# Kernel optimization log

Hardware: AMD Instinct MI355X
Metric: run time of the kernel (lower is better)

## Reference

```python
import jax, jax.numpy as jnp
import numpy as np

ENC = 512   # ENCODER_DIM / card embedding size / LSTM input size
CTX = 512   # context_embeddings width
H = 512     # LSTM hidden size
N = 100000  # num_cards


def _lstm_step(x, h, c, w_ih, w_hh, b_ih, b_hh):
    # PyTorch LSTM gate order: i, f, g, o
    gates = x @ w_ih.T + b_ih + h @ w_hh.T + b_hh
    i, f, g, o = jnp.split(gates, 4, axis=-1)
    c_new = jax.nn.sigmoid(f) * c + jax.nn.sigmoid(i) * jnp.tanh(g)
    h_new = jax.nn.sigmoid(o) * jnp.tanh(c_new)
    return h_new, c_new


def setup_inputs() -> dict:
    key = jax.random.key(0)
    ks = jax.random.split(key, 16)
    s = 0.05
    f32 = jnp.float32
    return {
        "context_embeddings": jax.random.normal(ks[0], (1, CTX), f32),
        "card_embeddings": jax.random.normal(ks[1], (N, ENC), f32),
        "eos_embedding": jax.random.normal(ks[2], (ENC,), f32) * 0.1,
        "ctx_w": jax.random.normal(ks[3], (ENC, CTX), f32) * s,
        "ctx_b": jnp.zeros((ENC,), f32),
        "out_w": jax.random.normal(ks[4], (ENC, H), f32) * s,
        "out_b": jnp.zeros((ENC,), f32),
        "w_ih_0": jax.random.normal(ks[5], (4 * H, ENC), f32) * s,
        "w_hh_0": jax.random.normal(ks[6], (4 * H, H), f32) * s,
        "b_ih_0": jnp.zeros((4 * H,), f32),
        "b_hh_0": jnp.zeros((4 * H,), f32),
        "w_ih_1": jax.random.normal(ks[7], (4 * H, H), f32) * s,
        "w_hh_1": jax.random.normal(ks[8], (4 * H, H), f32) * s,
        "b_ih_1": jnp.zeros((4 * H,), f32),
        "b_hh_1": jnp.zeros((4 * H,), f32),
        "max_selections": 5,
    }


def reference(context_embeddings, card_embeddings, eos_embedding,
              ctx_w, ctx_b, out_w, out_b,
              w_ih_0, w_hh_0, b_ih_0, b_hh_0,
              w_ih_1, w_hh_1, b_ih_1, b_hh_1,
              max_selections):
    temperature = 1.0
    num_cards = card_embeddings.shape[0]
    hid = w_hh_0.shape[1]
    dt = card_embeddings.dtype

    # initial LSTM step on projected context with zero state (seq_len == 1)
    x0 = context_embeddings @ ctx_w.T + ctx_b                     # [1, ENC]
    z = jnp.zeros((1, hid), dt)
    h0, c0 = _lstm_step(x0, z, z, w_ih_0, w_hh_0, b_ih_0, b_hh_0)
    h1, c1 = _lstm_step(h0, z, z, w_ih_1, w_hh_1, b_ih_1, b_hh_1)

    all_emb = jnp.concatenate([card_embeddings, eos_embedding[None, :]], axis=0)  # [N+1, ENC]
    avail = jnp.ones((num_cards,), bool)
    active = jnp.array(True)
    total_log_prob = jnp.asarray(0.0, dt)
    keys = jax.random.split(jax.random.key(42), max_selections)
    card_ids = jnp.arange(num_cards)

    indices = []
    n_steps = min(int(max_selections), num_cards)
    for step in range(n_steps):
        proj = h1 @ out_w.T + out_b                               # [1, ENC]
        card_sims = proj @ card_embeddings.T                      # [1, N]
        eos_sim = proj @ eos_embedding[:, None]                   # [1, 1]
        logits = jnp.concatenate([card_sims, eos_sim], axis=-1)[0] / temperature  # [N+1]
        ext_mask = jnp.concatenate([avail, jnp.ones((1,), bool)])
        logits = jnp.where(ext_mask, logits, -jnp.inf)

        idx = jax.random.categorical(keys[step], logits)          # multinomial(softmax(logits))
        log_prob = jax.nn.log_softmax(logits)[idx]
        total_log_prob = total_log_prob + jnp.where(active, log_prob, jnp.asarray(0.0, dt))

        is_eos = idx == num_cards
        take = active & (~is_eos)
        indices.append(jnp.where(take, idx, -1).astype(jnp.int32))
        avail = avail & ~((card_ids == idx) & take)

        # straight-through one-hot gather of the selected embedding
        hard = jax.nn.one_hot(idx, num_cards + 1, dtype=dt)
        soft = jax.nn.softmax(logits)
        ste = hard + soft - jax.lax.stop_gradient(soft)
        sel_emb = (ste @ all_emb)[None, :]                        # [1, ENC]

        h0, c0 = _lstm_step(sel_emb, h0, c0, w_ih_0, w_hh_0, b_ih_0, b_hh_0)
        h1, c1 = _lstm_step(h0, h1, c1, w_ih_1, w_hh_1, b_ih_1, b_hh_1)
        active = active & (~is_eos)

    selected_indices = jnp.stack(indices)                         # [max_selections], -1 = not selected
    return selected_indices, total_log_prob
```

## Files before the change

### kernel.cpp

```cpp
#include <hip/hip_runtime.h>
#include <stdint.h>
#include <math.h>

#define ENC 512
#define NSTEPS 5
#define NBLK 512
#define NTHR 256
#define NWAVES ((NBLK * NTHR) / 64)
#define ROWS_PER_ITER (NWAVES * 8)
#define FB_BLOCKS 1024
#define FB_WAVES (FB_BLOCKS * 256 / 64)
#define GSTRIDE 100032

struct SelState {
  int   taken[8];
  int   takenCount;
  int   active;
  int   outIdx[8];
  float tlp;
};

struct KParams {
  const float *ctx, *cards, *eos, *ctx_w, *ctx_b, *out_w, *out_b;
  const float *w_ih_0, *w_hh_0, *b_ih_0, *b_hh_0;
  const float *w_ih_1, *w_hh_1, *b_ih_1, *b_hh_1;
  unsigned* bar;
  float* xbuf;
  float* h0s; float* c0s; float* h1s; float* c1s;
  float* projs;
  SelState* st;
  float* bScore; int* bIdxA; float* bLogit; float* bM; float* bS;
  float* gtab;
  float* out;
  int ncards;
  uint32_t k0[NSTEPS], k1[NSTEPS];
};

__host__ __device__ __forceinline__ void tf2x32(uint32_t k0, uint32_t k1,
                                                uint32_t x0, uint32_t x1,
                                                uint32_t& o0, uint32_t& o1) {
  uint32_t ks0 = k0, ks1 = k1, ks2 = k0 ^ k1 ^ 0x1BD11BDAu;
  uint32_t ks[3] = {ks0, ks1, ks2};
  const uint32_t R0[4] = {13u, 15u, 26u, 6u};
  const uint32_t R1[4] = {17u, 29u, 16u, 24u};
  x0 += ks0; x1 += ks1;
#pragma unroll
  for (int i = 0; i < 5; ++i) {
    const uint32_t* r = (i & 1) ? R1 : R0;
#pragma unroll
    for (int j = 0; j < 4; ++j) {
      x0 += x1;
      x1 = (x1 << r[j]) | (x1 >> (32u - r[j]));
      x1 ^= x0;
    }
    x0 += ks[(i + 1) % 3];
    x1 += ks[(i + 2) % 3] + (uint32_t)(i + 1);
  }
  o0 = x0; o1 = x1;
}

__device__ __forceinline__ float gumbel_from_bits(uint32_t bits) {
  float f = __uint_as_float((bits >> 9) | 0x3F800000u) - 1.0f;
  float u = (f == 0.0f) ? 1.17549435e-38f : f;
  return -logf(-logf(u));
}

__device__ __forceinline__ float xla_tanh(float x) {
  if (fabsf(x) < 0.0004f) return x;
  const float kLim = 7.90531110763549805f;
  float cx = fminf(fmaxf(x, -kLim), kLim);
  float x2 = cx * cx;
  float p = -2.76076847742355e-16f;
  p = fmaf(p, x2, 2.00018790482477e-13f);
  p = fmaf(p, x2, -8.60467152213735e-11f);
  p = fmaf(p, x2, 5.12229709037114e-08f);
  p = fmaf(p, x2, 1.48572235717979e-05f);
  p = fmaf(p, x2, 6.37261928875436e-04f);
  p = fmaf(p, x2, 4.89352455891786e-03f);
  p = cx * p;
  float q = 1.19825839466702e-06f;
  q = fmaf(q, x2, 1.18534705686654e-04f);
  q = fmaf(q, x2, 2.26843463243900e-03f);
  q = fmaf(q, x2, 4.89352518554385e-03f);
  return p / q;
}
__device__ __forceinline__ float xla_sigmoid(float x) {
  return 0.5f * xla_tanh(0.5f * x) + 0.5f;
}

__device__ __forceinline__ float dot8(const float4* a, const float4* b, int lane) {
  float4 x0 = a[lane * 2], x1 = a[lane * 2 + 1];
  float4 y0 = b[lane * 2], y1 = b[lane * 2 + 1];
  return x0.x * y0.x + x0.y * y0.y + x0.z * y0.z + x0.w * y0.w +
         x1.x * y1.x + x1.y * y1.y + x1.z * y1.z + x1.w * y1.w;
}
__device__ __forceinline__ float wred(float v) {
#pragma unroll
  for (int k = 1; k < 64; k <<= 1) v += __shfl_xor(v, k, 64);
  return v;
}

__device__ __forceinline__ void cstoref(float* p, float v) {
  __hip_atomic_store(p, v, __ATOMIC_RELAXED, __HIP_MEMORY_SCOPE_AGENT);
}
__device__ __forceinline__ void cstorei(int* p, int v) {
  __hip_atomic_store(p, v, __ATOMIC_RELAXED, __HIP_MEMORY_SCOPE_AGENT);
}

__device__ __forceinline__ void arrive(unsigned* bar, int bid, unsigned target) {
  asm volatile("s_waitcnt vmcnt(0)" ::: "memory");
  __syncthreads();
  if (threadIdx.x == 0)
    __hip_atomic_store(&bar[(unsigned)bid * 16u], target,
                       __ATOMIC_RELAXED, __HIP_MEMORY_SCOPE_AGENT);
}
__device__ __forceinline__ void waitall(unsigned* bar, unsigned target) {
  const int tid = threadIdx.x;
  unsigned* s0 = &bar[(2u * (unsigned)tid) * 16u];
  unsigned* s1 = &bar[(2u * (unsigned)tid + 1u) * 16u];
  while (__hip_atomic_load(s0, __ATOMIC_RELAXED, __HIP_MEMORY_SCOPE_AGENT) < target)
    __builtin_amdgcn_s_sleep(1);
  while (__hip_atomic_load(s1, __ATOMIC_RELAXED, __HIP_MEMORY_SCOPE_AGENT) < target)
    __builtin_amdgcn_s_sleep(1);
  __syncthreads();
}
__device__ __forceinline__ void gsync(unsigned* bar, int bid, unsigned target) {
  arrive(bar, bid, target);
  waitall(bar, target);
}

__device__ __forceinline__ void lstm_phase(const float* wih, const float* whh,
                                           const float* bih, const float* bhh,
                                           const float* x, const float* hin, const float* cin,
                                           float* hout, float* cout, float* sG,
                                           int bid, int tid) {
  if (bid < ENC) {
    int g = tid >> 6, lane = tid & 63;
    size_t row = (size_t)(g * ENC + bid) * ENC;
    float accI = dot8((const float4*)(wih + row), (const float4*)x, lane);
    float accH = 0.0f;
    if (hin) accH = dot8((const float4*)(whh + row), (const float4*)hin, lane);
#pragma unroll
    for (int k = 1; k < 64; k <<= 1) {
      accI += __shfl_xor(accI, k, 64);
      accH += __shfl_xor(accH, k, 64);
    }
    if (lane == 0) sG[g] = ((accI + bih[g * ENC + bid]) + accH) + bhh[g * ENC + bid];
    __syncthreads();
    if (tid == 0) {
      float gi = sG[0], gf = sG[1], gg = sG[2], go = sG[3];
      float cprev = cin ? cin[bid] : 0.0f;
      float cn = xla_sigmoid(gf) * cprev + xla_sigmoid(gi) * xla_tanh(gg);
      float hn = xla_sigmoid(go) * xla_tanh(cn);
      cstoref(&cout[bid], cn);
      cstoref(&hout[bid], hn);
    }
  }
}

__global__ __launch_bounds__(NTHR, 2) void mega(KParams P) {
  const int bid = blockIdx.x, tid = threadIdx.x;
  const int wid = tid >> 6, lane = tid & 63;
  const int gw = bid * 4 + wid;
  const int sub = lane & 15;
  const int grp = lane >> 4;
  const int g = wid;
  unsigned ph = 0;

  __shared__ float sG[4];
  __shared__ float fS[NTHR], fL[NTHR], fM[NTHR], fU[NTHR];
  __shared__ int   fI[NTHR];
  __shared__ float wSs[16], wLs[16], wMs[16], wUs[16];
  __shared__ int   wIs[16];
  __shared__ int   sTaken[8];
  __shared__ int   sActive;
  __shared__ float sTlp;
  __shared__ int   sOut[NSTEPS];
  __shared__ int   selSh;

  if (tid == 0) {
    for (int i = 0; i < 8; ++i) sTaken[i] = -1;
    sActive = 1; sTlp = 0.0f;
    for (int i = 0; i < NSTEPS; ++i) sOut[i] = -1;
  }

  const int np1 = P.ncards + 1;
  const int ITERS = (np1 + ROWS_PER_ITER - 1) / ROWS_PER_ITER;

  {
    int total = NSTEPS * np1;
    for (int j = bid * NTHR + tid; j < total; j += NBLK * NTHR) {
      int s = j / np1;
      int i = j - s * np1;
      uint32_t r0, r1;
      tf2x32(P.k0[s], P.k1[s], 0u, (uint32_t)i, r0, r1);
      cstoref(&P.gtab[s * GSTRIDE + i], gumbel_from_bits(r0 ^ r1));
    }
  }
  if (gw >= NWAVES - ENC) {
    int r = gw - (NWAVES - ENC);
    float acc = wred(dot8((const float4*)(P.ctx_w + (size_t)r * ENC), (const float4*)P.ctx, lane));
    if (lane == 0) cstoref(&P.xbuf[r], acc + P.ctx_b[r]);
  }
  gsync(P.bar, bid, ++ph);

  lstm_phase(P.w_ih_0, P.w_hh_0, P.b_ih_0, P.b_hh_0, P.xbuf, nullptr, nullptr,
             P.h0s, P.c0s, sG, bid, tid);
  gsync(P.bar, bid, ++ph);
  lstm_phase(P.w_ih_1, P.w_hh_1, P.b_ih_1, P.b_hh_1, P.h0s, nullptr, nullptr,
             P.h1s, P.c1s, sG, bid, tid);
  gsync(P.bar, bid, ++ph);

  if (gw < ENC) {
    float acc = wred(dot8((const float4*)(P.out_w + (size_t)gw * ENC), (const float4*)P.h1s, lane));
    if (lane == 0) cstoref(&P.projs[gw], acc + P.out_b[gw]);
  }
  gsync(P.bar, bid, ++ph);

  for (int s = 0; s < NSTEPS; ++s) {
    {
      const float4* pv = (const float4*)(P.projs + s * ENC);
      float4 pr[8];
#pragma unroll
      for (int k = 0; k < 8; ++k) pr[k] = pv[sub + 16 * k];
      int t0 = sTaken[0], t1 = sTaken[1], t2 = sTaken[2], t3 = sTaken[3], t4 = sTaken[4];
      const float* gt = P.gtab + s * GSTRIDE;
      float bSc = -INFINITY, bLg = 0.0f, m = -INFINITY, su = 0.0f;
      int bIx = 0x7FFFFFFF;
      for (int t = 0; t < ITERS; ++t) {
        int base = (t * NWAVES + gw) * 8;
        int rA = base + grp;
        int rB = base + 4 + grp;
        bool vA = (rA < np1), vB = (rB < np1);
        const float* rpA = vA ? ((rA < P.ncards) ? (P.cards + (size_t)rA * ENC) : P.eos) : P.cards;
        const float* rpB = vB ? ((rB < P.ncards) ? (P.cards + (size_t)rB * ENC) : P.eos) : P.cards;
        const float4* ra = (const float4*)rpA;
        const float4* rb = (const float4*)rpB;
        float4 rrA[8], rrB[8];
#pragma unroll
        for (int k = 0; k < 8; ++k) { rrA[k] = ra[sub + 16 * k]; rrB[k] = rb[sub + 16 * k]; }
        float gA = vA ? gt[rA] : 0.0f;
        float gB = vB ? gt[rB] : 0.0f;
        float accA = 0.0f, accB = 0.0f;
#pragma unroll
        for (int k = 0; k < 8; ++k) {
          accA += rrA[k].x * pr[k].x + rrA[k].y * pr[k].y + rrA[k].z * pr[k].z + rrA[k].w * pr[k].w;
          accB += rrB[k].x * pr[k].x + rrB[k].y * pr[k].y + rrB[k].z * pr[k].z + rrB[k].w * pr[k].w;
        }
        accA += __shfl_xor(accA, 1, 64); accB += __shfl_xor(accB, 1, 64);
        accA += __shfl_xor(accA, 2, 64); accB += __shfl_xor(accB, 2, 64);
        accA += __shfl_xor(accA, 4, 64); accB += __shfl_xor(accB, 4, 64);
        accA += __shfl_xor(accA, 8, 64); accB += __shfl_xor(accB, 8, 64);
        if (sub == 0) {
          if (vA) {
            bool masked = (rA < P.ncards) &&
                          (rA == t0 || rA == t1 || rA == t2 || rA == t3 || rA == t4);
            if (!masked) {
              if (accA > m) { su = su * expf(m - accA) + 1.0f; m = accA; }
              else          { su += expf(accA - m); }
              float score = gA + accA;
              if (score > bSc || (score == bSc && rA < bIx)) { bSc = score; bIx = rA; bLg = accA; }
            }
          }
          if (vB) {
            bool masked = (rB < P.ncards) &&
                          (rB == t0 || rB == t1 || rB == t2 || rB == t3 || rB == t4);
            if (!masked) {
              if (accB > m) { su = su * expf(m - accB) + 1.0f; m = accB; }
              else          { su += expf(accB - m); }
              float score = gB + accB;
              if (score > bSc || (score == bSc && rB < bIx)) { bSc = score; bIx = rB; bLg = accB; }
            }
          }
        }
      }
      if (sub == 0) {
        int q = wid * 4 + grp;
        wSs[q] = bSc; wIs[q] = bIx; wLs[q] = bLg; wMs[q] = m; wUs[q] = su;
      }
      __syncthreads();
      if (tid == 0) {
        float s2 = wSs[0], l2 = wLs[0], m2 = wMs[0], u2 = wUs[0];
        int i2 = wIs[0];
        for (int k = 1; k < 16; ++k) {
          float cs = wSs[k]; int ci = wIs[k];
          if (cs > s2 || (cs == s2 && ci < i2)) { s2 = cs; i2 = ci; l2 = wLs[k]; }
          float cm = wMs[k], cu = wUs[k];
          if (cm > m2) { u2 = u2 * expf(m2 - cm) + cu; m2 = cm; }
          else if (cm > -INFINITY) { u2 += cu * expf(cm - m2); }
        }
        int o = s * NBLK + bid;
        cstoref(&P.bScore[o], s2); cstorei(&P.bIdxA[o], i2);
        cstoref(&P.bLogit[o], l2); cstoref(&P.bM[o], m2); cstoref(&P.bS[o], u2);
      }
    }
    arrive(P.bar, bid, ++ph);
    if (s == NSTEPS - 1 && bid != 0) return;

    float4 dwa, dwb, dva, dvb, dha, dhb;
    float dbi = 0.0f, dbh = 0.0f, dci = 0.0f;
    if (s < NSTEPS - 1) {
      size_t row = (size_t)(g * ENC + bid) * ENC;
      const float4* wi = (const float4*)(P.w_ih_0 + row);
      const float4* wh = (const float4*)(P.w_hh_0 + row);
      dwa = wi[lane * 2]; dwb = wi[lane * 2 + 1];
      dva = wh[lane * 2]; dvb = wh[lane * 2 + 1];
      const float4* hv = (const float4*)(P.h0s + s * ENC);
      dha = hv[lane * 2]; dhb = hv[lane * 2 + 1];
      dbi = P.b_ih_0[g * ENC + bid]; dbh = P.b_hh_0[g * ENC + bid];
      dci = P.c0s[s * ENC + bid];
    }
    waitall(P.bar, ph);

    {
      const float* pSc = P.bScore + s * NBLK;
      const int*   pIx = P.bIdxA  + s * NBLK;
      const float* pLg = P.bLogit + s * NBLK;
      const float* pMm = P.bM     + s * NBLK;
      const float* pSu = P.bS     + s * NBLK;
      float bS2 = -INFINITY, bL2 = 0.0f, m = -INFINITY, su = 0.0f;
      int bI2 = 0x7FFFFFFF;
      for (int i = tid; i < NBLK; i += NTHR) {
        float cs = pSc[i]; int ci = pIx[i];
        if (cs > bS2 || (cs == bS2 && ci < bI2)) { bS2 = cs; bI2 = ci; bL2 = pLg[i]; }
        float cm = pMm[i], cu = pSu[i];
        if (cm > m) { su = su * expf(m - cm) + cu; m = cm; }
        else if (cm > -INFINITY) { su += cu * expf(cm - m); }
      }
      fS[tid] = bS2; fI[tid] = bI2; fL[tid] = bL2; fM[tid] = m; fU[tid] = su;
      __syncthreads();
      for (int off = 128; off > 0; off >>= 1) {
        if (tid < off) {
          float cs = fS[tid + off]; int ci = fI[tid + off];
          if (cs > fS[tid] || (cs == fS[tid] && ci < fI[tid])) {
            fS[tid] = cs; fI[tid] = ci; fL[tid] = fL[tid + off];
          }
          float cm = fM[tid + off], cu = fU[tid + off];
          if (cm > fM[tid]) { fU[tid] = fU[tid] * expf(fM[tid] - cm) + cu; fM[tid] = cm; }
          else if (cm > -INFINITY) { fU[tid] += cu * expf(cm - fM[tid]); }
        }
        __syncthreads();
      }
      if (tid == 0) {
        int idx = fI[0];
        float lse = fM[0] + logf(fU[0]);
        float lp = fL[0] - lse;
        int active = sActive;
        if (active) sTlp += lp;
        int is_eos = (idx == P.ncards);
        int take = active && !is_eos;
        sOut[s] = take ? idx : -1;
        if (take) {
          for (int q = 0; q < 8; ++q) if (sTaken[q] == -1) { sTaken[q] = idx; break; }
        }
        sActive = active && !is_eos;
        selSh = idx;
        if (s == NSTEPS - 1 && bid == 0) {
          for (int q = 0; q < NSTEPS; ++q) P.out[q] = (float)sOut[q];
          P.out[NSTEPS] = sTlp;
        }
      }
      __syncthreads();
    }
    if (s == NSTEPS - 1) break;

    {
      int idx = selSh;
      const float* xrow = (idx < P.ncards) ? (P.cards + (size_t)idx * ENC) : P.eos;
      const float4* xv = (const float4*)xrow;
      float4 xa = xv[lane * 2], xb = xv[lane * 2 + 1];
      float accI = dwa.x * xa.x + dwa.y * xa.y + dwa.z * xa.z + dwa.w * xa.w +
                   dwb.x * xb.x + dwb.y * xb.y + dwb.z * xb.z + dwb.w * xb.w;
      float accH = dva.x * dha.x + dva.y * dha.y + dva.z * dha.z + dva.w * dha.w +
                   dvb.x * dhb.x + dvb.y * dhb.y + dvb.z * dhb.z + dvb.w * dhb.w;
#pragma unroll
      for (int k = 1; k < 64; k <<= 1) {
        accI += __shfl_xor(accI, k, 64);
        accH += __shfl_xor(accH, k, 64);
      }
      if (lane == 0) sG[g] = ((accI + dbi) + accH) + dbh;
      __syncthreads();
      if (tid == 0) {
        float gi = sG[0], gf = sG[1], gg = sG[2], go = sG[3];
        float cn = xla_sigmoid(gf) * dci + xla_sigmoid(gi) * xla_tanh(gg);
        float hn = xla_sigmoid(go) * xla_tanh(cn);
        cstoref(&P.c0s[(s + 1) * ENC + bid], cn);
        cstoref(&P.h0s[(s + 1) * ENC + bid], hn);
      }
    }
    arrive(P.bar, bid, ++ph);
    float4 ewa, ewb, eva, evb, eha, ehb;
    float ebi, ebh, eci;
    {
      size_t row = (size_t)(g * ENC + bid) * ENC;
      const float4* wi = (const float4*)(P.w_ih_1 + row);
      const float4* wh = (const float4*)(P.w_hh_1 + row);
      ewa = wi[lane * 2]; ewb = wi[lane * 2 + 1];
      eva = wh[lane * 2]; evb = wh[lane * 2 + 1];
      const float4* hv = (const float4*)(P.h1s + s * ENC);
      eha = hv[lane * 2]; ehb = hv[lane * 2 + 1];
      ebi = P.b_ih_1[g * ENC + bid]; ebh = P.b_hh_1[g * ENC + bid];
      eci = P.c1s[s * ENC + bid];
    }
    waitall(P.bar, ph);

    {
      const float4* xv = (const float4*)(P.h0s + (s + 1) * ENC);
      float4 xa = xv[lane * 2], xb = xv[lane * 2 + 1];
      float accI = ewa.x * xa.x + ewa.y * xa.y + ewa.z * xa.z + ewa.w * xa.w +
                   ewb.x * xb.x + ewb.y * xb.y + ewb.z * xb.z + ewb.w * xb.w;
      float accH = eva.x * eha.x + eva.y * eha.y + eva.z * eha.z + eva.w * eha.w +
                   evb.x * ehb.x + evb.y * ehb.y + evb.z * ehb.z + evb.w * ehb.w;
#pragma unroll
      for (int k = 1; k < 64; k <<= 1) {
        accI += __shfl_xor(accI, k, 64);
        accH += __shfl_xor(accH, k, 64);
      }
      if (lane == 0) sG[g] = ((accI + ebi) + accH) + ebh;
      __syncthreads();
      if (tid == 0) {
        float gi = sG[0], gf = sG[1], gg = sG[2], go = sG[3];
        float cn = xla_sigmoid(gf) * eci + xla_sigmoid(gi) * xla_tanh(gg);
        float hn = xla_sigmoid(go) * xla_tanh(cn);
        cstoref(&P.c1s[(s + 1) * ENC + bid], cn);
        cstoref(&P.h1s[(s + 1) * ENC + bid], hn);
      }
    }
    arrive(P.bar, bid, ++ph);
    float4 awa, awb;
    if (gw < ENC) {
      const float4* ow = (const float4*)(P.out_w + (size_t)gw * ENC);
      awa = ow[lane * 2]; awb = ow[lane * 2 + 1];
    }
    waitall(P.bar, ph);

    if (gw < ENC) {
      const float4* hv = (const float4*)(P.h1s + (s + 1) * ENC);
      float4 ha = hv[lane * 2], hb = hv[lane * 2 + 1];
      float acc = awa.x * ha.x + awa.y * ha.y + awa.z * ha.z + awa.w * ha.w +
                  awb.x * hb.x + awb.y * hb.y + awb.z * hb.z + awb.w * hb.w;
      acc = wred(acc);
      if (lane == 0) cstoref(&P.projs[(s + 1) * ENC + gw], acc + P.out_b[gw]);
    }
    gsync(P.bar, bid, ++ph);
  }
}

__global__ void init_kernel(float* __restrict__ Z, SelState* st) {
  int t = threadIdx.x;
  if (t < ENC) Z[t] = 0.0f;
  if (t == 0) {
    for (int i = 0; i < 8; ++i) { st->taken[i] = -1; st->outIdx[i] = -1; }
    st->takenCount = 0; st->active = 1; st->tlp = 0.0f;
  }
}

__global__ void gumbel_fill(float* __restrict__ gtab, int ncards,
                            uint32_t k00, uint32_t k01, uint32_t k10, uint32_t k11,
                            uint32_t k20, uint32_t k21, uint32_t k30, uint32_t k31,
                            uint32_t k40, uint32_t k41) {
  uint32_t K0[NSTEPS] = {k00, k10, k20, k30, k40};
  uint32_t K1[NSTEPS] = {k01, k11, k21, k31, k41};
  int np1 = ncards + 1;
  int total = NSTEPS * np1;
  for (int j = blockIdx.x * blockDim.x + threadIdx.x; j < total; j += gridDim.x * blockDim.x) {
    int s = j / np1;
    int i = j - s * np1;
    uint32_t r0, r1;
    tf2x32(K0[s], K1[s], 0u, (uint32_t)i, r0, r1);
    gtab[s * GSTRIDE + i] = gumbel_from_bits(r0 ^ r1);
  }
}

__global__ void matvec512(const float* __restrict__ W, const float* __restrict__ b,
                          const float* __restrict__ vin, float* __restrict__ vout) {
  int tid = blockIdx.x * blockDim.x + threadIdx.x;
  int wave = tid >> 6, lane = tid & 63;
  if (wave >= ENC) return;
  float acc = wred(dot8((const float4*)(W + (size_t)wave * ENC), (const float4*)vin, lane));
  if (lane == 0) vout[wave] = acc + b[wave];
}

__global__ void lstm_step_kernel(const float* __restrict__ w_ih, const float* __restrict__ w_hh,
                                 const float* __restrict__ b_ih, const float* __restrict__ b_hh,
                                 const float* __restrict__ x, const float* __restrict__ h_in,
                                 const float* __restrict__ c_in,
                                 float* __restrict__ h_out, float* __restrict__ c_out) {
  __shared__ float sG[4];
  lstm_phase(w_ih, w_hh, b_ih, b_hh, x, h_in, c_in, h_out, c_out, sG,
             blockIdx.x, threadIdx.x);
}

__global__ void sims_kernel(const float* __restrict__ cards, const float* __restrict__ eos,
                            const float* __restrict__ proj, int ncards,
                            const float* __restrict__ gt,
                            const int* __restrict__ takenList,
                            float* __restrict__ oScore, int* __restrict__ oIdx,
                            float* __restrict__ oLogit, float* __restrict__ oM,
                            float* __restrict__ oS) {
  int tid = blockIdx.x * blockDim.x + threadIdx.x;
  int wave = tid >> 6, lane = tid & 63;
  int nwav = (gridDim.x * blockDim.x) >> 6;
  const float4* pv = (const float4*)proj;
  float4 p0 = pv[lane * 2], p1 = pv[lane * 2 + 1];
  int t0 = takenList[0], t1 = takenList[1], t2 = takenList[2],
      t3 = takenList[3], t4 = takenList[4];
  float bS = -INFINITY, bL = 0.0f, m = -INFINITY, s = 0.0f;
  int bI = 0x7FFFFFFF;
  for (int i = wave; i <= ncards; i += nwav) {
    const float* rowp = (i < ncards) ? (cards + (size_t)i * ENC) : eos;
    const float4* er = (const float4*)rowp;
    float4 e0 = er[lane * 2], e1 = er[lane * 2 + 1];
    float acc = p0.x * e0.x + p0.y * e0.y + p0.z * e0.z + p0.w * e0.w +
                p1.x * e1.x + p1.y * e1.y + p1.z * e1.z + p1.w * e1.w;
    acc = wred(acc);
    bool masked = (i < ncards) &&
                  (i == t0 || i == t1 || i == t2 || i == t3 || i == t4);
    if (!masked) {
      if (acc > m) { s = s * expf(m - acc) + 1.0f; m = acc; }
      else         { s += expf(acc - m); }
      float score = gt[i] + acc;
      if (score > bS || (score == bS && i < bI)) { bS = score; bI = i; bL = acc; }
    }
  }
  if (lane == 0) { oScore[wave] = bS; oIdx[wave] = bI; oLogit[wave] = bL; oM[wave] = m; oS[wave] = s; }
}

__global__ void finalize_kernel(int nw, int step, int ncards,
                                const float* __restrict__ pScore, const int* __restrict__ pIdx,
                                const float* __restrict__ pLogit, const float* __restrict__ pM,
                                const float* __restrict__ pS,
                                const float* __restrict__ cards, const float* __restrict__ eos,
                                SelState* st, float* __restrict__ xout,
                                float* __restrict__ out, int write_out) {
  __shared__ float sS[256], sL[256], sM[256], sU[256];
  __shared__ int sI[256];
  __shared__ int selIdx;
  int t = threadIdx.x;
  float bS = -INFINITY, bL = 0.0f, m = -INFINITY, s = 0.0f;
  int bI = 0x7FFFFFFF;
  for (int i = t; i < nw; i += 256) {
    float cs = pScore[i]; int ci = pIdx[i];
    if (cs > bS || (cs == bS && ci < bI)) { bS = cs; bI = ci; bL = pLogit[i]; }
    float cm = pM[i], cu = pS[i];
    if (cm > m) { s = s * expf(m - cm) + cu; m = cm; }
    else if (cm > -INFINITY) { s += cu * expf(cm - m); }
  }
  sS[t] = bS; sI[t] = bI; sL[t] = bL; sM[t] = m; sU[t] = s;
  __syncthreads();
  for (int off = 128; off > 0; off >>= 1) {
    if (t < off) {
      float cs = sS[t + off]; int ci = sI[t + off];
      if (cs > sS[t] || (cs == sS[t] && ci < sI[t])) { sS[t] = cs; sI[t] = ci; sL[t] = sL[t + off]; }
      float cm = sM[t + off], cu = sU[t + off];
      if (cm > sM[t]) { sU[t] = sU[t] * expf(sM[t] - cm) + cu; sM[t] = cm; }
      else if (cm > -INFINITY) { sU[t] += cu * expf(cm - sM[t]); }
    }
    __syncthreads();
  }
  if (t == 0) {
    int idx = sI[0];
    float lse = sM[0] + logf(sU[0]);
    float lp = sL[0] - lse;
    int active = st->active;
    if (active) st->tlp += lp;
    int is_eos = (idx == ncards);
    int take = active && !is_eos;
    st->outIdx[step] = take ? idx : -1;
    if (take) st->taken[st->takenCount++] = idx;
    st->active = active && !is_eos;
    selIdx = idx;
    if (write_out) {
      for (int q = 0; q < NSTEPS; ++q) out[q] = (float)st->outIdx[q];
      out[NSTEPS] = st->tlp;
    }
  }
  __syncthreads();
  if (!write_out) {
    int idx = selIdx;
    const float* row = (idx < ncards) ? (cards + (size_t)idx * ENC) : eos;
    for (int e = t; e < ENC; e += 256) xout[e] = row[e];
  }
}

extern "C" void kernel_launch(void* const* d_in, const int* in_sizes, int n_in,
                              void* d_out, int out_size, void* d_ws, size_t ws_size,
                              hipStream_t stream) {
  KParams P;
  P.ctx    = (const float*)d_in[0];
  P.cards  = (const float*)d_in[1];
  P.eos    = (const float*)d_in[2];
  P.ctx_w  = (const float*)d_in[3];
  P.ctx_b  = (const float*)d_in[4];
  P.out_w  = (const float*)d_in[5];
  P.out_b  = (const float*)d_in[6];
  P.w_ih_0 = (const float*)d_in[7];
  P.w_hh_0 = (const float*)d_in[8];
  P.b_ih_0 = (const float*)d_in[9];
  P.b_hh_0 = (const float*)d_in[10];
  P.w_ih_1 = (const float*)d_in[11];
  P.w_hh_1 = (const float*)d_in[12];
  P.b_ih_1 = (const float*)d_in[13];
  P.b_hh_1 = (const float*)d_in[14];
  P.ncards = in_sizes[1] / ENC;

  char* wsb = (char*)d_ws;
  P.bar = (unsigned*)wsb;
  float* f = (float*)(wsb + 40960);
  float* Z = f; f += ENC;
  P.xbuf = f; f += ENC;
  P.h0s = f; f += 6 * ENC;
  P.c0s = f; f += 6 * ENC;
  P.h1s = f; f += 6 * ENC;
  P.c1s = f; f += 6 * ENC;
  P.projs = f; f += NSTEPS * ENC;
  P.st = (SelState*)f;  f = (float*)((char*)f + 256);
  P.bScore = f; f += FB_WAVES;
  P.bIdxA = (int*)f; f += FB_WAVES;
  P.bLogit = f; f += FB_WAVES;
  P.bM = f; f += FB_WAVES;
  P.bS = f; f += FB_WAVES;
  P.gtab = f;
  P.out = (float*)d_out;

  for (int s = 0; s < NSTEPS; ++s)
    tf2x32(0u, 42u, 0u, (uint32_t)s, P.k0[s], P.k1[s]);

  hipMemsetAsync(P.bar, 0, 40960, stream);

  void* args[] = { &P };
  hipError_t ce = hipLaunchCooperativeKernel((void*)mega, dim3(NBLK), dim3(NTHR), args, 0, stream);
  if (ce == hipSuccess) return;
  (void)hipGetLastError();

  float* h0A = P.h0s;            float* h0B = P.h0s + ENC;
  float* c0A = P.c0s;            float* c0B = P.c0s + ENC;
  float* h1A = P.h1s;            float* h1B = P.h1s + ENC;
  float* c1A = P.c1s;            float* c1B = P.c1s + ENC;
  float* proj = P.projs;
  float* xbuf = P.xbuf;

  init_kernel<<<1, 512, 0, stream>>>(Z, P.st);
  gumbel_fill<<<512, 256, 0, stream>>>(P.gtab, P.ncards,
                                       P.k0[0], P.k1[0], P.k0[1], P.k1[1], P.k0[2], P.k1[2],
                                       P.k0[3], P.k1[3], P.k0[4], P.k1[4]);
  matvec512<<<128, 256, 0, stream>>>(P.ctx_w, P.ctx_b, P.ctx, xbuf);
  lstm_step_kernel<<<512, 256, 0, stream>>>(P.w_ih_0, P.w_hh_0, P.b_ih_0, P.b_hh_0,
                                            xbuf, Z, Z, h0A, c0A);
  lstm_step_kernel<<<512, 256, 0, stream>>>(P.w_ih_1, P.w_hh_1, P.b_ih_1, P.b_hh_1,
                                            h0A, Z, Z, h1A, c1A);
  float *h0c = h0A, *c0c = c0A, *h1c = h1A, *c1c = c1A;
  float *h0n = h0B, *c0n = c0B, *h1n = h1B, *c1n = c1B;
  for (int s = 0; s < NSTEPS; ++s) {
    matvec512<<<128, 256, 0, stream>>>(P.out_w, P.out_b, h1c, proj);
    sims_kernel<<<FB_BLOCKS, 256, 0, stream>>>(P.cards, P.eos, proj, P.ncards,
                                               P.gtab + s * GSTRIDE, (const int*)P.st,
                                               P.bScore, P.bIdxA, P.bLogit, P.bM, P.bS);
    finalize_kernel<<<1, 256, 0, stream>>>(FB_WAVES, s, P.ncards,
                                           P.bScore, P.bIdxA, P.bLogit, P.bM, P.bS,
                                           P.cards, P.eos, P.st, xbuf,
                                           P.out, (s == NSTEPS - 1) ? 1 : 0);
    if (s == NSTEPS - 1) break;
    lstm_step_kernel<<<512, 256, 0, stream>>>(P.w_ih_0, P.w_hh_0, P.b_ih_0, P.b_hh_0,
                                              xbuf, h0c, c0c, h0n, c0n);
    lstm_step_kernel<<<512, 256, 0, stream>>>(P.w_ih_1, P.w_hh_1, P.b_ih_1, P.b_hh_1,
                                              h0n, h1c, c1c, h1n, c1n);
    float* tp;
    tp = h0c; h0c = h0n; h0n = tp;
    tp = c0c; c0c = c0n; c0n = tp;
    tp = h1c; h1c = h1n; h1n = tp;
    tp = c1c; c1c = c1n; c1n = tp;
  }
}
```

Measured before the change: 312.9 us.

## Confine LSTM/projection phases to 128 blocks with sub-grid barriers and flag broadcasts

Replaces the full 512-block grid barriers around the small LSTM and projection phases. Only 128 master blocks compute these phases, each handling four hidden columns, and they sync through a two-level 128-block barrier. The remaining blocks wait on a step flag. Block 0 alone reduces the per-block argmax/softmax partials and broadcasts the chosen index through a flag. The Gumbel fill is remapped so each wave writes the rows it will later scan. This cuts the number of blocks in each barrier, in exchange for serialising more LSTM work per block and making the final reduction depend on a single block.

Measured after the change: 303.5 us. 1.03x faster.

```diff
diff --git a/kernel.cpp b/kernel.cpp
--- a/kernel.cpp
+++ b/kernel.cpp
@@ -6,18 +6,23 @@
 #define NSTEPS 5
 #define NBLK 512
 #define NTHR 256
-#define NWAVES ((NBLK * NTHR) / 64)
-#define ROWS_PER_ITER (NWAVES * 8)
+#define NWAVES 2048
+#define RPI (NWAVES * 8)
+#define NMAST 128
+#define GSTRIDE 100032
 #define FB_BLOCKS 1024
-#define FB_WAVES (FB_BLOCKS * 256 / 64)
-#define GSTRIDE 100032
+#define FB_WAVES 4096
+
+#define OFF_SLOT   0
+#define OFF_SLOT1  8192
+#define OFF_REL1   10240
+#define OFF_CFLAG  10752
+#define OFF_STEPF  11776
+#define OFF_SELS   12800
+#define BAR_BYTES  53248
 
 struct SelState {
-  int   taken[8];
-  int   takenCount;
-  int   active;
-  int   outIdx[8];
-  float tlp;
+  int taken[8]; int takenCount; int active; int outIdx[8]; float tlp;
 };
 
 struct KParams {
@@ -99,34 +104,61 @@
   for (int k = 1; k < 64; k <<= 1) v += __shfl_xor(v, k, 64);
   return v;
 }
-
 __device__ __forceinline__ void cstoref(float* p, float v) {
   __hip_atomic_store(p, v, __ATOMIC_RELAXED, __HIP_MEMORY_SCOPE_AGENT);
 }
 __device__ __forceinline__ void cstorei(int* p, int v) {
   __hip_atomic_store(p, v, __ATOMIC_RELAXED, __HIP_MEMORY_SCOPE_AGENT);
 }
-
-__device__ __forceinline__ void arrive(unsigned* bar, int bid, unsigned target) {
+__device__ __forceinline__ unsigned cload(unsigned* p) {
+  return __hip_atomic_load(p, __ATOMIC_RELAXED, __HIP_MEMORY_SCOPE_AGENT);
+}
+
+__device__ __forceinline__ void arrive_slot(unsigned* slot_base, int idx, unsigned v) {
   asm volatile("s_waitcnt vmcnt(0)" ::: "memory");
   __syncthreads();
-  if (threadIdx.x == 0)
-    __hip_atomic_store(&bar[(unsigned)bid * 16u], target,
+  if (threadIdx.x == 0) __hip_atomic_store(&slot_base[(unsigned)idx * 16u], v,
+                                           __ATOMIC_RELAXED, __HIP_MEMORY_SCOPE_AGENT);
+}
+__device__ __forceinline__ void waitfull(unsigned* slots, unsigned v) {
+  unsigned* s0 = &slots[(2u * (unsigned)threadIdx.x) * 16u];
+  unsigned* s1 = &slots[(2u * (unsigned)threadIdx.x + 1u) * 16u];
+  while (cload(s0) < v) __builtin_amdgcn_s_sleep(2);
+  while (cload(s1) < v) __builtin_amdgcn_s_sleep(2);
+  __syncthreads();
+}
+__device__ __forceinline__ void wait128(unsigned* slots1, unsigned v) {
+  if (threadIdx.x < NMAST) {
+    unsigned* s = &slots1[(unsigned)threadIdx.x * 16u];
+    while (cload(s) < v) __builtin_amdgcn_s_sleep(1);
+  }
+  __syncthreads();
+}
+__device__ __forceinline__ void rel128_set(unsigned* rel1, unsigned v) {
+  if (threadIdx.x < 32)
+    __hip_atomic_store(&rel1[(unsigned)threadIdx.x * 16u], v,
                        __ATOMIC_RELAXED, __HIP_MEMORY_SCOPE_AGENT);
 }
-__device__ __forceinline__ void waitall(unsigned* bar, unsigned target) {
-  const int tid = threadIdx.x;
-  unsigned* s0 = &bar[(2u * (unsigned)tid) * 16u];
-  unsigned* s1 = &bar[(2u * (unsigned)tid + 1u) * 16u];
-  while (__hip_atomic_load(s0, __ATOMIC_RELAXED, __HIP_MEMORY_SCOPE_AGENT) < target)
-    __builtin_amdgcn_s_sleep(1);
-  while (__hip_atomic_load(s1, __ATOMIC_RELAXED, __HIP_MEMORY_SCOPE_AGENT) < target)
-    __builtin_amdgcn_s_sleep(1);
-  __syncthreads();
-}
-__device__ __forceinline__ void gsync(unsigned* bar, int bid, unsigned target) {
-  arrive(bar, bid, target);
-  waitall(bar, target);
+__device__ __forceinline__ void rel128_wait(unsigned* rel1, int bid, unsigned v) {
+  if (threadIdx.x == 0) {
+    unsigned* r = &rel1[((unsigned)bid & 31u) * 16u];
+    while (cload(r) < v) __builtin_amdgcn_s_sleep(1);
+  }
+  __syncthreads();
+}
+__device__ __forceinline__ void setflag(unsigned* flag, unsigned v) {
+  asm volatile("s_waitcnt vmcnt(0)" ::: "memory");
+  __syncthreads();
+  if (threadIdx.x < 64)
+    __hip_atomic_store(&flag[(unsigned)threadIdx.x * 16u], v,
+                       __ATOMIC_RELAXED, __HIP_MEMORY_SCOPE_AGENT);
+}
+__device__ __forceinline__ void flagwait(unsigned* flag, int bid, unsigned v) {
+  if (threadIdx.x == 0) {
+    unsigned* r = &flag[((unsigned)bid & 63u) * 16u];
+    while (cload(r) < v) __builtin_amdgcn_s_sleep(4);
+  }
+  __syncthreads();
 }
 
 __device__ __forceinline__ void lstm_phase(const float* wih, const float* whh,
@@ -162,60 +194,133 @@
   const int bid = blockIdx.x, tid = threadIdx.x;
   const int wid = tid >> 6, lane = tid & 63;
   const int gw = bid * 4 + wid;
-  const int sub = lane & 15;
-  const int grp = lane >> 4;
-  const int g = wid;
-  unsigned ph = 0;
-
-  __shared__ float sG[4];
+  const int sub = lane & 15, grp = lane >> 4;
+
+  unsigned* slots  = P.bar + OFF_SLOT;
+  unsigned* slots1 = P.bar + OFF_SLOT1;
+  unsigned* rel1   = P.bar + OFF_REL1;
+  unsigned* cflag  = P.bar + OFF_CFLAG;
+  unsigned* stepf  = P.bar + OFF_STEPF;
+  int*      selS   = (int*)(P.bar + OFF_SELS);
+
+  __shared__ float sGm[4][4];
   __shared__ float fS[NTHR], fL[NTHR], fM[NTHR], fU[NTHR];
   __shared__ int   fI[NTHR];
   __shared__ float wSs[16], wLs[16], wMs[16], wUs[16];
   __shared__ int   wIs[16];
-  __shared__ int   sTaken[8];
+  __shared__ int   tkSh[5];
+  __shared__ int   tkCnt;
+  __shared__ int   selX;
   __shared__ int   sActive;
   __shared__ float sTlp;
   __shared__ int   sOut[NSTEPS];
-  __shared__ int   selSh;
 
   if (tid == 0) {
-    for (int i = 0; i < 8; ++i) sTaken[i] = -1;
+    tkCnt = 0;
+    for (int i = 0; i < 5; ++i) tkSh[i] = -1;
     sActive = 1; sTlp = 0.0f;
     for (int i = 0; i < NSTEPS; ++i) sOut[i] = -1;
   }
+  __syncthreads();
 
   const int np1 = P.ncards + 1;
-  const int ITERS = (np1 + ROWS_PER_ITER - 1) / ROWS_PER_ITER;
+  const int ITERS = (np1 + RPI - 1) / RPI;
 
   {
-    int total = NSTEPS * np1;
-    for (int j = bid * NTHR + tid; j < total; j += NBLK * NTHR) {
-      int s = j / np1;
-      int i = j - s * np1;
-      uint32_t r0, r1;
-      tf2x32(P.k0[s], P.k1[s], 0u, (uint32_t)i, r0, r1);
-      cstoref(&P.gtab[s * GSTRIDE + i], gumbel_from_bits(r0 ^ r1));
-    }
-  }
-  if (gw >= NWAVES - ENC) {
-    int r = gw - (NWAVES - ENC);
-    float acc = wred(dot8((const float4*)(P.ctx_w + (size_t)r * ENC), (const float4*)P.ctx, lane));
-    if (lane == 0) cstoref(&P.xbuf[r], acc + P.ctx_b[r]);
-  }
-  gsync(P.bar, bid, ++ph);
-
-  lstm_phase(P.w_ih_0, P.w_hh_0, P.b_ih_0, P.b_hh_0, P.xbuf, nullptr, nullptr,
-             P.h0s, P.c0s, sG, bid, tid);
-  gsync(P.bar, bid, ++ph);
-  lstm_phase(P.w_ih_1, P.w_hh_1, P.b_ih_1, P.b_hh_1, P.h0s, nullptr, nullptr,
-             P.h1s, P.c1s, sG, bid, tid);
-  gsync(P.bar, bid, ++ph);
-
-  if (gw < ENC) {
-    float acc = wred(dot8((const float4*)(P.out_w + (size_t)gw * ENC), (const float4*)P.h1s, lane));
-    if (lane == 0) cstoref(&P.projs[gw], acc + P.out_b[gw]);
-  }
-  gsync(P.bar, bid, ++ph);
+    int s = lane >> 3, k = lane & 7;
+    if (s < NSTEPS) {
+      for (int t = 0; t < ITERS; ++t) {
+        int r = (t * NWAVES + gw) * 8 + k;
+        if (r < np1) {
+          uint32_t r0, r1;
+          tf2x32(P.k0[s], P.k1[s], 0u, (uint32_t)r, r0, r1);
+          P.gtab[s * GSTRIDE + r] = gumbel_from_bits(r0 ^ r1);
+        }
+      }
+    }
+  }
+
+  auto lstm_cols = [&](const float* wih, const float* whh,
+                       const float* bih, const float* bhh,
+                       const float* x, const float* hin, const float* cin,
+                       float* hout, float* cout) {
+    const float4* xv = (const float4*)x;
+    float4 xa = xv[lane * 2], xb = xv[lane * 2 + 1];
+    float4 ha, hb;
+    if (hin) {
+      const float4* hv = (const float4*)hin;
+      ha = hv[lane * 2]; hb = hv[lane * 2 + 1];
+    }
+    for (int j = 0; j < 4; ++j) {
+      int col = bid * 4 + j;
+      size_t row = (size_t)(wid * ENC + col) * ENC;
+      const float4* wi = (const float4*)(wih + row);
+      float4 a0 = wi[lane * 2], a1 = wi[lane * 2 + 1];
+      float accI = a0.x * xa.x + a0.y * xa.y + a0.z * xa.z + a0.w * xa.w +
+                   a1.x * xb.x + a1.y * xb.y + a1.z * xb.z + a1.w * xb.w;
+      float accH = 0.0f;
+      if (hin) {
+        const float4* wh = (const float4*)(whh + row);
+        float4 b0 = wh[lane * 2], b1 = wh[lane * 2 + 1];
+        accH = b0.x * ha.x + b0.y * ha.y + b0.z * ha.z + b0.w * ha.w +
+               b1.x * hb.x + b1.y * hb.y + b1.z * hb.z + b1.w * hb.w;
+      }
+#pragma unroll
+      for (int k = 1; k < 64; k <<= 1) {
+        accI += __shfl_xor(accI, k, 64);
+        accH += __shfl_xor(accH, k, 64);
+      }
+      if (lane == 0) sGm[wid][j] = ((accI + bih[wid * ENC + col]) + accH) + bhh[wid * ENC + col];
+    }
+    __syncthreads();
+    if (tid < 4) {
+      int col = bid * 4 + tid;
+      float gi = sGm[0][tid], gf = sGm[1][tid], gg = sGm[2][tid], go = sGm[3][tid];
+      float cprev = cin ? cin[col] : 0.0f;
+      float cn = xla_sigmoid(gf) * cprev + xla_sigmoid(gi) * xla_tanh(gg);
+      float hn = xla_sigmoid(go) * xla_tanh(cn);
+      cstoref(&cout[col], cn);
+      cstoref(&hout[col], hn);
+    }
+    __syncthreads();
+  };
+  auto proj_phase = [&](const float* h1, float* dst) {
+    const float4* ow = (const float4*)(P.out_w + (size_t)gw * ENC);
+    float acc = wred(dot8(ow, (const float4*)h1, lane));
+    if (lane == 0) cstoref(&dst[gw], acc + P.out_b[gw]);
+  };
+
+  unsigned b128 = 0;
+  if (bid < NMAST) {
+    {
+      const float4* cw = (const float4*)(P.ctx_w + (size_t)gw * ENC);
+      float acc = wred(dot8(cw, (const float4*)P.ctx, lane));
+      if (lane == 0) cstoref(&P.xbuf[gw], acc + P.ctx_b[gw]);
+    }
+    arrive_slot(slots1, bid, ++b128);
+    if (bid == 0) { wait128(slots1, b128); rel128_set(rel1, b128); }
+    else rel128_wait(rel1, bid, b128);
+    if (bid == 0) __syncthreads();
+
+    lstm_cols(P.w_ih_0, P.w_hh_0, P.b_ih_0, P.b_hh_0, P.xbuf, nullptr, nullptr, P.h0s, P.c0s);
+    arrive_slot(slots1, bid, ++b128);
+    if (bid == 0) { wait128(slots1, b128); rel128_set(rel1, b128); }
+    else rel128_wait(rel1, bid, b128);
+    if (bid == 0) __syncthreads();
+
+    lstm_cols(P.w_ih_1, P.w_hh_1, P.b_ih_1, P.b_hh_1, P.h0s, nullptr, nullptr, P.h1s, P.c1s);
+    arrive_slot(slots1, bid, ++b128);
+    if (bid == 0) { wait128(slots1, b128); rel128_set(rel1, b128); }
+    else rel128_wait(rel1, bid, b128);
+    if (bid == 0) __syncthreads();
+
+    proj_phase(P.h1s, P.projs);
+    arrive_slot(slots1, bid, ++b128);
+    if (bid == 0) { wait128(slots1, b128); setflag(stepf, 1); }
+  } else {
+    b128 = 4;
+  }
+  flagwait(stepf, bid, 1);
 
   for (int s = 0; s < NSTEPS; ++s) {
     {
@@ -223,7 +328,7 @@
       float4 pr[8];
 #pragma unroll
       for (int k = 0; k < 8; ++k) pr[k] = pv[sub + 16 * k];
-      int t0 = sTaken[0], t1 = sTaken[1], t2 = sTaken[2], t3 = sTaken[3], t4 = sTaken[4];
+      int t0 = tkSh[0], t1 = tkSh[1], t2 = tkSh[2], t3 = tkSh[3], t4 = tkSh[4];
       const float* gt = P.gtab + s * GSTRIDE;
       float bSc = -INFINITY, bLg = 0.0f, m = -INFINITY, su = 0.0f;
       int bIx = 0x7FFFFFFF;
@@ -294,25 +399,11 @@
         cstoref(&P.bLogit[o], l2); cstoref(&P.bM[o], m2); cstoref(&P.bS[o], u2);
       }
     }
-    arrive(P.bar, bid, ++ph);
+    arrive_slot(slots, bid, (unsigned)(s + 1));
     if (s == NSTEPS - 1 && bid != 0) return;
 
-    float4 dwa, dwb, dva, dvb, dha, dhb;
-    float dbi = 0.0f, dbh = 0.0f, dci = 0.0f;
-    if (s < NSTEPS - 1) {
-      size_t row = (size_t)(g * ENC + bid) * ENC;
-      const float4* wi = (const float4*)(P.w_ih_0 + row);
-      const float4* wh = (const float4*)(P.w_hh_0 + row);
-      dwa = wi[lane * 2]; dwb = wi[lane * 2 + 1];
-      dva = wh[lane * 2]; dvb = wh[lane * 2 + 1];
-      const float4* hv = (const float4*)(P.h0s + s * ENC);
-      dha = hv[lane * 2]; dhb = hv[lane * 2 + 1];
-      dbi = P.b_ih_0[g * ENC + bid]; dbh = P.b_hh_0[g * ENC + bid];
-      dci = P.c0s[s * ENC + bid];
-    }
-    waitall(P.bar, ph);
-
-    {
+    if (bid == 0) {
+      waitfull(slots, (unsigned)(s + 1));
       const float* pSc = P.bScore + s * NBLK;
       const int*   pIx = P.bIdxA  + s * NBLK;
       const float* pLg = P.bLogit + s * NBLK;
@@ -350,99 +441,62 @@
         int is_eos = (idx == P.ncards);
         int take = active && !is_eos;
         sOut[s] = take ? idx : -1;
-        if (take) {
-          for (int q = 0; q < 8; ++q) if (sTaken[q] == -1) { sTaken[q] = idx; break; }
-        }
         sActive = active && !is_eos;
-        selSh = idx;
-        if (s == NSTEPS - 1 && bid == 0) {
+        if (s == NSTEPS - 1) {
           for (int q = 0; q < NSTEPS; ++q) P.out[q] = (float)sOut[q];
           P.out[NSTEPS] = sTlp;
+        } else {
+          cstorei(&selS[s * 16], idx);
+          cstorei(&selS[s * 16 + 1], take ? idx : -1);
         }
       }
       __syncthreads();
-    }
-    if (s == NSTEPS - 1) break;
-
-    {
-      int idx = selSh;
-      const float* xrow = (idx < P.ncards) ? (P.cards + (size_t)idx * ENC) : P.eos;
-      const float4* xv = (const float4*)xrow;
-      float4 xa = xv[lane * 2], xb = xv[lane * 2 + 1];
-      float accI = dwa.x * xa.x + dwa.y * xa.y + dwa.z * xa.z + dwa.w * xa.w +
-                   dwb.x * xb.x + dwb.y * xb.y + dwb.z * xb.z + dwb.w * xb.w;
-      float accH = dva.x * dha.x + dva.y * dha.y + dva.z * dha.z + dva.w * dha.w +
-                   dvb.x * dhb.x + dvb.y * dhb.y + dvb.z * dhb.z + dvb.w * dhb.w;
-#pragma unroll
-      for (int k = 1; k < 64; k <<= 1) {
-        accI += __shfl_xor(accI, k, 64);
-        accH += __shfl_xor(accH, k, 64);
-      }
-      if (lane == 0) sG[g] = ((accI + dbi) + accH) + dbh;
+      if (s == NSTEPS - 1) return;
+      setflag(cflag, (unsigned)(s + 1));
+    }
+
+    if (bid < NMAST) {
+      flagwait(cflag, bid, (unsigned)(s + 1));
+      if (tid == 0) {
+        int xI = selS[s * 16];
+        int tI = selS[s * 16 + 1];
+        selX = xI;
+        if (tI >= 0) tkSh[tkCnt++] = tI;
+      }
       __syncthreads();
+      {
+        int idx = selX;
+        const float* xrow = (idx < P.ncards) ? (P.cards + (size_t)idx * ENC) : P.eos;
+        lstm_cols(P.w_ih_0, P.w_hh_0, P.b_ih_0, P.b_hh_0, xrow,
+                  P.h0s + s * ENC, P.c0s + s * ENC,
+                  P.h0s + (s + 1) * ENC, P.c0s + (s + 1) * ENC);
+      }
+      arrive_slot(slots1, bid, ++b128);
+      if (bid == 0) { wait128(slots1, b128); rel128_set(rel1, b128); }
+      else rel128_wait(rel1, bid, b128);
+      if (bid == 0) __syncthreads();
+
+      lstm_cols(P.w_ih_1, P.w_hh_1, P.b_ih_1, P.b_hh_1, P.h0s + (s + 1) * ENC,
+                P.h1s + s * ENC, P.c1s + s * ENC,
+                P.h1s + (s + 1) * ENC, P.c1s + (s + 1) * ENC);
+      arrive_slot(slots1, bid, ++b128);
+      if (bid == 0) { wait128(slots1, b128); rel128_set(rel1, b128); }
+      else rel128_wait(rel1, bid, b128);
+      if (bid == 0) __syncthreads();
+
+      proj_phase(P.h1s + (s + 1) * ENC, P.projs + (s + 1) * ENC);
+      arrive_slot(slots1, bid, ++b128);
+      if (bid == 0) { wait128(slots1, b128); setflag(stepf, (unsigned)(s + 2)); }
+      flagwait(stepf, bid, (unsigned)(s + 2));
+    } else {
+      b128 += 3;
+      flagwait(stepf, bid, (unsigned)(s + 2));
       if (tid == 0) {
-        float gi = sG[0], gf = sG[1], gg = sG[2], go = sG[3];
-        float cn = xla_sigmoid(gf) * dci + xla_sigmoid(gi) * xla_tanh(gg);
-        float hn = xla_sigmoid(go) * xla_tanh(cn);
-        cstoref(&P.c0s[(s + 1) * ENC + bid], cn);
-        cstoref(&P.h0s[(s + 1) * ENC + bid], hn);
-      }
-    }
-    arrive(P.bar, bid, ++ph);
-    float4 ewa, ewb, eva, evb, eha, ehb;
-    float ebi, ebh, eci;
-    {
-      size_t row = (size_t)(g * ENC + bid) * ENC;
-      const float4* wi = (const float4*)(P.w_ih_1 + row);
-      const float4* wh = (const float4*)(P.w_hh_1 + row);
-      ewa = wi[lane * 2]; ewb = wi[lane * 2 + 1];
-      eva = wh[lane * 2]; evb = wh[lane * 2 + 1];
-      const float4* hv = (const float4*)(P.h1s + s * ENC);
-      eha = hv[lane * 2]; ehb = hv[lane * 2 + 1];
-      ebi = P.b_ih_1[g * ENC + bid]; ebh = P.b_hh_1[g * ENC + bid];
-      eci = P.c1s[s * ENC + bid];
-    }
-    waitall(P.bar, ph);
-
-    {
-      const float4* xv = (const float4*)(P.h0s + (s + 1) * ENC);
-      float4 xa = xv[lane * 2], xb = xv[lane * 2 + 1];
-      float accI = ewa.x * xa.x + ewa.y * xa.y + ewa.z * xa.z + ewa.w * xa.w +
-                   ewb.x * xb.x + ewb.y * xb.y + ewb.z * xb.z + ewb.w * xb.w;
-      float accH = eva.x * eha.x + eva.y * eha.y + eva.z * eha.z + eva.w * eha.w +
-                   evb.x * ehb.x + evb.y * ehb.y + evb.z * ehb.z + evb.w * ehb.w;
-#pragma unroll
-      for (int k = 1; k < 64; k <<= 1) {
-        accI += __shfl_xor(accI, k, 64);
-        accH += __shfl_xor(accH, k, 64);
-      }
-      if (lane == 0) sG[g] = ((accI + ebi) + accH) + ebh;
+        int tI = selS[s * 16 + 1];
+        if (tI >= 0) tkSh[tkCnt++] = tI;
+      }
       __syncthreads();
-      if (tid == 0) {
-        float gi = sG[0], gf = sG[1], gg = sG[2], go = sG[3];
-        float cn = xla_sigmoid(gf) * eci + xla_sigmoid(gi) * xla_tanh(gg);
-        float hn = xla_sigmoid(go) * xla_tanh(cn);
-        cstoref(&P.c1s[(s + 1) * ENC + bid], cn);
-        cstoref(&P.h1s[(s + 1) * ENC + bid], hn);
-      }
-    }
-    arrive(P.bar, bid, ++ph);
-    float4 awa, awb;
-    if (gw < ENC) {
-      const float4* ow = (const float4*)(P.out_w + (size_t)gw * ENC);
-      awa = ow[lane * 2]; awb = ow[lane * 2 + 1];
-    }
-    waitall(P.bar, ph);
-
-    if (gw < ENC) {
-      const float4* hv = (const float4*)(P.h1s + (s + 1) * ENC);
-      float4 ha = hv[lane * 2], hb = hv[lane * 2 + 1];
-      float acc = awa.x * ha.x + awa.y * ha.y + awa.z * ha.z + awa.w * ha.w +
-                  awb.x * hb.x + awb.y * hb.y + awb.z * hb.z + awb.w * hb.w;
-      acc = wred(acc);
-      if (lane == 0) cstoref(&P.projs[(s + 1) * ENC + gw], acc + P.out_b[gw]);
-    }
-    gsync(P.bar, bid, ++ph);
+    }
   }
 }
 
@@ -606,7 +660,7 @@
 
   char* wsb = (char*)d_ws;
   P.bar = (unsigned*)wsb;
-  float* f = (float*)(wsb + 40960);
+  float* f = (float*)(wsb + BAR_BYTES);
   float* Z = f; f += ENC;
   P.xbuf = f; f += ENC;
   P.h0s = f; f += 6 * ENC;
@@ -626,7 +680,7 @@
   for (int s = 0; s < NSTEPS; ++s)
     tf2x32(0u, 42u, 0u, (uint32_t)s, P.k0[s], P.k1[s]);
 
-  hipMemsetAsync(P.bar, 0, 40960, stream);
+  hipMemsetAsync(P.bar, 0, BAR_BYTES, stream);
 
   void* args[] = { &P };
   hipError_t ce = hipLaunchCooperativeKernel((void*)mega, dim3(NBLK), dim3(NTHR), args, 0, stream);
```
